# Optimization experiments

Measured on AMD Instinct MI355X. Metric: run time of the kernel, lower is better.

The kernel has to match this reference:

```python
import jax, jax.numpy as jnp
import numpy as np

H = 12          # num heads
D = 768         # embed dim
HD = D // H     # head dim
SCALE = HD ** -0.5
NEG = -(3.0 ** 39)  # matches torch's triu(1) * -3.0**39 mask value


def setup_inputs() -> dict:
    key = jax.random.key(0)
    ks = jax.random.split(key, 9)
    B, S = 4, 1024
    lim = 1.0 / np.sqrt(D)
    def lin(k):
        kw, kb = jax.random.split(k)
        W = jax.random.uniform(kw, (D, D), jnp.float32, -lim, lim)  # [out,in]
        b = jax.random.uniform(kb, (D,), jnp.float32, -lim, lim)
        return W, b
    Wq, bq = lin(ks[0]); Wk, bk = lin(ks[1]); Wv, bv = lin(ks[2]); Wo, bo = lin(ks[3])
    hidden_states = jax.random.normal(ks[4], (B, S, D), jnp.float32)
    return {"hidden_states": hidden_states,
            "Wq": Wq, "bq": bq, "Wk": Wk, "bk": bk,
            "Wv": Wv, "bv": bv, "Wo": Wo, "bo": bo}


def reference(hidden_states, Wq, bq, Wk, bk, Wv, bv, Wo, bo):
    B, S, _ = hidden_states.shape
    split = lambda x: x.reshape(B, S, H, HD).transpose(0, 2, 1, 3)  # [B,H,S,HD]
    q = split(hidden_states @ Wq.T + bq) * SCALE
    k = split(hidden_states @ Wk.T + bk)
    v = split(hidden_states @ Wv.T + bv)
    scores = jnp.einsum('bhqd,bhkd->bhqk', q, k)
    causal_mask = jnp.triu(jnp.full((S, S), NEG, hidden_states.dtype), k=1)
    scores = scores + causal_mask  # broadcast over [B,H]
    probs = jax.nn.softmax(scores, axis=-1)
    out = jnp.einsum('bhqk,bhkd->bhqd', probs, v)
    out = out.transpose(0, 2, 1, 3).reshape(B, S, H * HD)
    return out @ Wo.T + bo
```

## Files before the change

kernel.cpp:

```cpp
#include <hip/hip_runtime.h>

#define NH 12
#define DM 768
#define HD 64
#define BB 4
#define SS 1024
#define MTOT (BB*SS)
#define ATT_SCALE 0.125f
#define NEGMASK (-4.0525551530189755e18f)

typedef __attribute__((ext_vector_type(8))) short short8;
typedef __attribute__((ext_vector_type(4))) float floatx4;
typedef __attribute__((ext_vector_type(4))) unsigned short ushort4v;

__device__ __forceinline__ float bf2f(unsigned short u){
    union { unsigned int i; float f; } x; x.i = ((unsigned int)u) << 16; return x.f;
}
__device__ __forceinline__ unsigned short f2bf(float f){
    union { float f; unsigned int i; } x; x.f = f;
    unsigned int i = x.i;
    return (unsigned short)((i + 0x7FFFu + ((i >> 16) & 1u)) >> 16);
}

#define XQ4 (MTOT*DM/4)
#define WQ4 (DM*DM/4)

__global__ __launch_bounds__(256) void convert_bf16(
    const float* __restrict__ X,
    const float* __restrict__ Wq, const float* __restrict__ Wk,
    const float* __restrict__ Wv, const float* __restrict__ Wo,
    unsigned short* __restrict__ Xb,
    unsigned short* __restrict__ Wqb, unsigned short* __restrict__ Wkb,
    unsigned short* __restrict__ Wvb, unsigned short* __restrict__ Wob)
{
    const int idx = blockIdx.x * 256 + threadIdx.x;
    const float* s; unsigned short* d; int off;
    if (idx < XQ4) { s = X; d = Xb; off = idx; }
    else {
        const int r = idx - XQ4;
        const int wsel = r / WQ4;
        off = r - wsel * WQ4;
        s = (wsel==0)?Wq:(wsel==1)?Wk:(wsel==2)?Wv:Wo;
        d = (wsel==0)?Wqb:(wsel==1)?Wkb:(wsel==2)?Wvb:Wob;
    }
    const float4 v = ((const float4*)s)[off];
    ushort4v o;
    o[0] = f2bf(v.x); o[1] = f2bf(v.y); o[2] = f2bf(v.z); o[3] = f2bf(v.w);
    ((ushort4v*)d)[off] = o;
}

__device__ __forceinline__ void gemm_stage(
    const unsigned short* __restrict__ A,
    const unsigned short* __restrict__ Bm,
    int m0, int n0, int k0, int w, int lane,
    unsigned short* __restrict__ As, unsigned short* __restrict__ Bs)
{
    const int srow = lane >> 2;
    const int ske  = (lane & 3) * 8;
    #pragma unroll
    for (int j = 0; j < 2; ++j) {
        const int row = w*32 + j*16 + srow;
        __builtin_amdgcn_global_load_lds(
            (const __attribute__((address_space(1))) unsigned int*)
                (A + (size_t)(m0 + row) * DM + k0 + ske),
            (__attribute__((address_space(3))) unsigned int*)
                (As + (w*32 + j*16) * 32),
            16, 0, 0);
        __builtin_amdgcn_global_load_lds(
            (const __attribute__((address_space(1))) unsigned int*)
                (Bm + (size_t)(n0 + row) * DM + k0 + ske),
            (__attribute__((address_space(3))) unsigned int*)
                (Bs + (w*32 + j*16) * 32),
            16, 0, 0);
    }
}

__device__ __forceinline__ void gemm_compute(
    const unsigned short* __restrict__ As,
    const unsigned short* __restrict__ Bs,
    int wr, int wc, int c, int g, floatx4 (&acc)[4][4])
{
    short8 af[4], bfr[4];
    #pragma unroll
    for (int mi = 0; mi < 4; ++mi)
        af[mi] = *(const short8*)(As + (wr*64 + mi*16 + c)*32 + g*8);
    #pragma unroll
    for (int ni = 0; ni < 4; ++ni)
        bfr[ni] = *(const short8*)(Bs + (wc*64 + ni*16 + c)*32 + g*8);
    #pragma unroll
    for (int mi = 0; mi < 4; ++mi)
        #pragma unroll
        for (int ni = 0; ni < 4; ++ni)
            acc[mi][ni] = __builtin_amdgcn_mfma_f32_16x16x32_bf16(
                af[mi], bfr[ni], acc[mi][ni], 0, 0, 0);
}

__global__ __launch_bounds__(256) void qkv_mfma(
    const unsigned short* __restrict__ Xb,
    const unsigned short* __restrict__ Wqkv,
    const float* __restrict__ bq, const float* __restrict__ bk,
    const float* __restrict__ bv,
    unsigned short* __restrict__ qout,
    unsigned short* __restrict__ kout,
    unsigned short* __restrict__ vout)
{
    const int bx = blockIdx.x;
    const int which = bx / 6;
    const int np0 = (bx % 6) * 128;
    const int n0 = bx * 128;
    const int m0 = blockIdx.y * 128;

    const float* bias = (which==0) ? bq : (which==1) ? bk : bv;
    const float scl = (which==0) ? ATT_SCALE : 1.0f;

    __shared__ unsigned short As[2][128*32];
    __shared__ unsigned short Bs[2][128*32];

    const int t = threadIdx.x;
    const int w = t >> 6, lane = t & 63;
    const int c = lane & 15, g = lane >> 4;
    const int wr = w >> 1, wc = w & 1;

    floatx4 acc[4][4] = {};

    gemm_stage(Xb, Wqkv, m0, n0, 0, w, lane, As[0], Bs[0]);
    __syncthreads();

    #pragma unroll 2
    for (int kt = 0; kt < 24; ++kt) {
        const int cur = kt & 1;
        if (kt + 1 < 24)
            gemm_stage(Xb, Wqkv, m0, n0, (kt+1)*32, w, lane, As[cur^1], Bs[cur^1]);
        gemm_compute(As[cur], Bs[cur], wr, wc, c, g, acc);
        if (kt + 1 < 24)
            __syncthreads();
    }

    #pragma unroll
    for (int mi = 0; mi < 4; ++mi) {
        #pragma unroll
        for (int r = 0; r < 4; ++r) {
            const int m = m0 + wr*64 + mi*16 + g*4 + r;
            const int b = m >> 10, s = m & 1023;
            #pragma unroll
            for (int ni = 0; ni < 4; ++ni) {
                const int np = np0 + wc*64 + ni*16 + c;
                const int h = np >> 6, hd = np & 63;
                const float val = (acc[mi][ni][r] + bias[np]) * scl;
                if (which == 2)
                    vout[(((size_t)(b*NH + h))*HD + hd)*SS + s] = f2bf(val);
                else if (which == 1)
                    kout[(((size_t)(b*NH + h))*SS + s)*HD + hd] = f2bf(val);
                else
                    qout[(((size_t)(b*NH + h))*SS + s)*HD + hd] = f2bf(val);
            }
        }
    }
}

__device__ __forceinline__ void stage_tile(
    const unsigned short* __restrict__ Kp,
    const unsigned short* __restrict__ VTp,
    int k0, int w, int lane,
    unsigned short* __restrict__ Ks,
    unsigned short* __restrict__ Vs)
{
    const int rsub = lane >> 3;
    const int cc   = (lane & 7) ^ rsub;
    #pragma unroll
    for (int j = 0; j < 2; ++j) {
        const int r = w*16 + j*8 + rsub;
        __builtin_amdgcn_global_load_lds(
            (const __attribute__((address_space(1))) unsigned int*)
                (Kp + (size_t)(k0 + r) * HD + cc*8),
            (__attribute__((address_space(3))) unsigned int*)
                (Ks + (w*16 + j*8) * HD),
            16, 0, 0);
        __builtin_amdgcn_global_load_lds(
            (const __attribute__((address_space(1))) unsigned int*)
                (VTp + (size_t)r * SS + k0 + cc*8),
            (__attribute__((address_space(3))) unsigned int*)
                (Vs + (w*16 + j*8) * HD),
            16, 0, 0);
    }
}

__device__ __forceinline__ void attn_process_tile(
    const unsigned short* __restrict__ Ks,
    const unsigned short* __restrict__ Vs,
    const short8 (&qf)[2],
    int k0, bool islast, int qg, int c, int g,
    float& m_c, float& l_c, floatx4 (&Oacc)[4],
    unsigned short* __restrict__ Pl)
{
    floatx4 S[4] = {};
    #pragma unroll
    for (int nf = 0; nf < 4; ++nf) {
        const int row = nf*16 + c;
        #pragma unroll
        for (int st = 0; st < 2; ++st) {
            const short8 kf = *(const short8*)(Ks + row*HD + (((g + 4*st) ^ (c & 7)) * 8));
            S[nf] = __builtin_amdgcn_mfma_f32_16x16x32_bf16(kf, qf[st], S[nf], 0, 0, 0);
        }
    }

    if (islast) {
        #pragma unroll
        for (int nf = 0; nf < 4; ++nf) {
            #pragma unroll
            for (int r = 0; r < 4; ++r) {
                const int key = k0 + nf*16 + g*4 + r;
                if (key > qg) S[nf][r] += NEGMASK;
            }
        }
    }

    float mx = -INFINITY;
    #pragma unroll
    for (int nf = 0; nf < 4; ++nf)
        #pragma unroll
        for (int r = 0; r < 4; ++r) mx = fmaxf(mx, S[nf][r]);
    mx = fmaxf(mx, __shfl_xor(mx, 16, 64));
    mx = fmaxf(mx, __shfl_xor(mx, 32, 64));
    const float mnew = fmaxf(m_c, mx);
    const float alpha = __expf(m_c - mnew);
    float sum = 0.0f;
    #pragma unroll
    for (int nf = 0; nf < 4; ++nf)
        #pragma unroll
        for (int r = 0; r < 4; ++r) {
            const float p = __expf(S[nf][r] - mnew);
            S[nf][r] = p;
            sum += p;
        }
    sum += __shfl_xor(sum, 16, 64);
    sum += __shfl_xor(sum, 32, 64);
    l_c = l_c * alpha + sum;
    m_c = mnew;
    #pragma unroll
    for (int nf = 0; nf < 4; ++nf)
        #pragma unroll
        for (int r = 0; r < 4; ++r) Oacc[nf][r] *= alpha;

    #pragma unroll
    for (int nf = 0; nf < 4; ++nf)
        #pragma unroll
        for (int r = 0; r < 4; ++r)
            Pl[c * 72 + nf*16 + g*4 + r] = f2bf(S[nf][r]);

    #pragma unroll
    for (int st = 0; st < 2; ++st) {
        const short8 pf = *(const short8*)(Pl + c * 72 + g*8 + 32*st);
        #pragma unroll
        for (int nf = 0; nf < 4; ++nf) {
            const int row = nf*16 + c;
            const short8 vf = *(const short8*)(Vs + row*HD + (((g + 4*st) ^ (c & 7)) * 8));
            Oacc[nf] = __builtin_amdgcn_mfma_f32_16x16x32_bf16(vf, pf, Oacc[nf], 0, 0, 0);
        }
    }
}

__global__ __launch_bounds__(256) void attn_mfma(
    const unsigned short* __restrict__ Q,
    const unsigned short* __restrict__ K,
    const unsigned short* __restrict__ VT,
    unsigned short* __restrict__ O)
{
    const int idx = blockIdx.x;
    const int bh  = idx % 48;
    const int z   = 15 - (idx / 48);
    const int q0  = z * 64;

    const unsigned short* Qp  = Q  + (size_t)bh * SS * HD;
    const unsigned short* Kp  = K  + (size_t)bh * SS * HD;
    const unsigned short* VTp = VT + (size_t)bh * HD * SS;

    __shared__ unsigned short Ks[2][64*HD];
    __shared__ unsigned short Vs[2][64*HD];
    __shared__ unsigned short Pl[4][16*72];

    const int t    = threadIdx.x;
    const int w    = t >> 6;
    const int lane = t & 63;
    const int c    = lane & 15;
    const int g    = lane >> 4;
    const int qg   = q0 + w*16 + c;

    short8 qf[2];
    #pragma unroll
    for (int st = 0; st < 2; ++st)
        qf[st] = *(const short8*)(Qp + (size_t)qg * HD + g*8 + 32*st);

    floatx4 Oacc[4] = {};
    float m_c = -INFINITY, l_c = 0.0f;

    const int ntile = z + 1;

    stage_tile(Kp, VTp, 0, w, lane, Ks[0], Vs[0]);
    __syncthreads();

    for (int kt = 0; kt < ntile; ++kt) {
        const int cur = kt & 1;
        if (kt + 1 < ntile)
            stage_tile(Kp, VTp, (kt+1)*64, w, lane, Ks[cur^1], Vs[cur^1]);
        attn_process_tile(Ks[cur], Vs[cur], qf, kt*64, kt == ntile-1,
                          qg, c, g, m_c, l_c, Oacc, Pl[w]);
        if (kt + 1 < ntile)
            __syncthreads();
    }

    const int b = bh / NH, h = bh % NH;
    const float inv = 1.0f / l_c;
    unsigned short* op = O + ((size_t)(b*SS + qg))*DM + h*HD;
    #pragma unroll
    for (int nf = 0; nf < 4; ++nf) {
        ushort4v o4;
        #pragma unroll
        for (int r = 0; r < 4; ++r) o4[r] = f2bf(Oacc[nf][r] * inv);
        *(ushort4v*)(op + nf*16 + g*4) = o4;
    }
}

__global__ __launch_bounds__(256) void out_mfma(
    const unsigned short* __restrict__ A,
    const unsigned short* __restrict__ Wb,
    const float* __restrict__ bias,
    float* __restrict__ outf)
{
    const int n0 = blockIdx.x * 128;
    const int m0 = blockIdx.y * 128;

    __shared__ unsigned short As[2][128*32];
    __shared__ unsigned short Bs[2][128*32];

    const int t = threadIdx.x;
    const int w = t >> 6, lane = t & 63;
    const int c = lane & 15, g = lane >> 4;
    const int wr = w >> 1, wc = w & 1;

    floatx4 acc[4][4] = {};

    gemm_stage(A, Wb, m0, n0, 0, w, lane, As[0], Bs[0]);
    __syncthreads();

    #pragma unroll 2
    for (int kt = 0; kt < 24; ++kt) {
        const int cur = kt & 1;
        if (kt + 1 < 24)
            gemm_stage(A, Wb, m0, n0, (kt+1)*32, w, lane, As[cur^1], Bs[cur^1]);
        gemm_compute(As[cur], Bs[cur], wr, wc, c, g, acc);
        if (kt + 1 < 24)
            __syncthreads();
    }

    #pragma unroll
    for (int mi = 0; mi < 4; ++mi) {
        #pragma unroll
        for (int r = 0; r < 4; ++r) {
            const int m = m0 + wr*64 + mi*16 + g*4 + r;
            #pragma unroll
            for (int ni = 0; ni < 4; ++ni) {
                const int n = n0 + wc*64 + ni*16 + c;
                outf[(size_t)m * DM + n] = acc[mi][ni][r] + bias[n];
            }
        }
    }
}

extern "C" void kernel_launch(void* const* d_in, const int* in_sizes, int n_in,
                              void* d_out, int out_size, void* d_ws, size_t ws_size,
                              hipStream_t stream) {
    const float* X  = (const float*)d_in[0];
    const float* Wq = (const float*)d_in[1];
    const float* bq = (const float*)d_in[2];
    const float* Wk = (const float*)d_in[3];
    const float* bk = (const float*)d_in[4];
    const float* Wv = (const float*)d_in[5];
    const float* bv = (const float*)d_in[6];
    const float* Wo = (const float*)d_in[7];
    const float* bo = (const float*)d_in[8];
    float* out = (float*)d_out;

    const size_t elems = (size_t)MTOT * DM;
    const size_t welems = (size_t)DM * DM;
    unsigned short* q    = (unsigned short*)d_ws;
    unsigned short* k    = q    + elems;
    unsigned short* vt   = k    + elems;
    unsigned short* attn = vt   + elems;
    unsigned short* xb   = attn + elems;
    unsigned short* wqb  = xb   + elems;
    unsigned short* wkb  = wqb  + welems;
    unsigned short* wvb  = wkb  + welems;
    unsigned short* wob  = wvb  + welems;

    convert_bf16<<<dim3((XQ4 + 4*WQ4) / 256), 256, 0, stream>>>(
        X, Wq, Wk, Wv, Wo, xb, wqb, wkb, wvb, wob);
    qkv_mfma<<<dim3(18, 32), 256, 0, stream>>>(
        xb, wqb, bq, bk, bv, q, k, vt);
    attn_mfma<<<dim3(768), 256, 0, stream>>>(q, k, vt, attn);
    out_mfma<<<dim3(6, 32), 256, 0, stream>>>(attn, wob, bo, out);
}
```

Measured before the change: 177.1 us.

## Retile projection GEMMs to 128x64 with BK=64 swizzled LDS, vectorize P stores

The QKV and output projection GEMMs move from 128x128 tiles with BK=32 double buffering to 128x64 tiles with BK=64, single-buffered, using an XOR-swizzled LDS layout. This doubles the grid size so more blocks fill the CUs, and it should reduce LDS bank conflicts on fragment reads. The cost is the loss of load/compute overlap from double buffering and lower per-block reuse. The attention kernel also packs its P-tile LDS writes into 4-wide vector stores.

```diff
diff --git a/kernel.cpp b/kernel.cpp
--- a/kernel.cpp
+++ b/kernel.cpp
@@ -49,50 +49,57 @@
     ((ushort4v*)d)[off] = o;
 }
 
-__device__ __forceinline__ void gemm_stage(
+__device__ __forceinline__ void gemm_stage64(
     const unsigned short* __restrict__ A,
     const unsigned short* __restrict__ Bm,
     int m0, int n0, int k0, int w, int lane,
-    unsigned short* __restrict__ As, unsigned short* __restrict__ Bs)
-{
-    const int srow = lane >> 2;
-    const int ske  = (lane & 3) * 8;
-    #pragma unroll
-    for (int j = 0; j < 2; ++j) {
-        const int row = w*32 + j*16 + srow;
+    unsigned short* __restrict__ As,
+    unsigned short* __restrict__ Bs)
+{
+    const int rsub = lane >> 3;
+    const int cc   = (lane & 7) ^ rsub;
+    #pragma unroll
+    for (int j = 0; j < 4; ++j) {
+        const int rb = w*32 + j*8;
         __builtin_amdgcn_global_load_lds(
             (const __attribute__((address_space(1))) unsigned int*)
-                (A + (size_t)(m0 + row) * DM + k0 + ske),
-            (__attribute__((address_space(3))) unsigned int*)
-                (As + (w*32 + j*16) * 32),
+                (A + (size_t)(m0 + rb + rsub) * DM + k0 + cc*8),
+            (__attribute__((address_space(3))) unsigned int*)(As + rb*64),
             16, 0, 0);
+    }
+    #pragma unroll
+    for (int j = 0; j < 2; ++j) {
+        const int rb = w*16 + j*8;
         __builtin_amdgcn_global_load_lds(
             (const __attribute__((address_space(1))) unsigned int*)
-                (Bm + (size_t)(n0 + row) * DM + k0 + ske),
-            (__attribute__((address_space(3))) unsigned int*)
-                (Bs + (w*32 + j*16) * 32),
+                (Bm + (size_t)(n0 + rb + rsub) * DM + k0 + cc*8),
+            (__attribute__((address_space(3))) unsigned int*)(Bs + rb*64),
             16, 0, 0);
     }
 }
 
-__device__ __forceinline__ void gemm_compute(
+__device__ __forceinline__ void gemm_compute64(
     const unsigned short* __restrict__ As,
     const unsigned short* __restrict__ Bs,
-    int wr, int wc, int c, int g, floatx4 (&acc)[4][4])
-{
-    short8 af[4], bfr[4];
-    #pragma unroll
-    for (int mi = 0; mi < 4; ++mi)
-        af[mi] = *(const short8*)(As + (wr*64 + mi*16 + c)*32 + g*8);
-    #pragma unroll
-    for (int ni = 0; ni < 4; ++ni)
-        bfr[ni] = *(const short8*)(Bs + (wc*64 + ni*16 + c)*32 + g*8);
-    #pragma unroll
-    for (int mi = 0; mi < 4; ++mi)
-        #pragma unroll
-        for (int ni = 0; ni < 4; ++ni)
-            acc[mi][ni] = __builtin_amdgcn_mfma_f32_16x16x32_bf16(
-                af[mi], bfr[ni], acc[mi][ni], 0, 0, 0);
+    int wr, int wc, int c, int g, floatx4 (&acc)[4][2])
+{
+    #pragma unroll
+    for (int st = 0; st < 2; ++st) {
+        const int chunk = ((g + 4*st) ^ (c & 7)) * 8;
+        short8 af[4], bfr[2];
+        #pragma unroll
+        for (int mi = 0; mi < 4; ++mi)
+            af[mi] = *(const short8*)(As + (wr*64 + mi*16 + c)*64 + chunk);
+        #pragma unroll
+        for (int ni = 0; ni < 2; ++ni)
+            bfr[ni] = *(const short8*)(Bs + (wc*32 + ni*16 + c)*64 + chunk);
+        #pragma unroll
+        for (int mi = 0; mi < 4; ++mi)
+            #pragma unroll
+            for (int ni = 0; ni < 2; ++ni)
+                acc[mi][ni] = __builtin_amdgcn_mfma_f32_16x16x32_bf16(
+                    af[mi], bfr[ni], acc[mi][ni], 0, 0, 0);
+    }
 }
 
 __global__ __launch_bounds__(256) void qkv_mfma(
@@ -105,35 +112,29 @@
     unsigned short* __restrict__ vout)
 {
     const int bx = blockIdx.x;
-    const int which = bx / 6;
-    const int np0 = (bx % 6) * 128;
-    const int n0 = bx * 128;
+    const int which = bx / 12;
+    const int np0 = (bx % 12) * 64;
+    const int n0 = bx * 64;
     const int m0 = blockIdx.y * 128;
 
     const float* bias = (which==0) ? bq : (which==1) ? bk : bv;
     const float scl = (which==0) ? ATT_SCALE : 1.0f;
 
-    __shared__ unsigned short As[2][128*32];
-    __shared__ unsigned short Bs[2][128*32];
+    __shared__ unsigned short As[128*64];
+    __shared__ unsigned short Bs[64*64];
 
     const int t = threadIdx.x;
     const int w = t >> 6, lane = t & 63;
     const int c = lane & 15, g = lane >> 4;
     const int wr = w >> 1, wc = w & 1;
 
-    floatx4 acc[4][4] = {};
-
-    gemm_stage(Xb, Wqkv, m0, n0, 0, w, lane, As[0], Bs[0]);
-    __syncthreads();
-
-    #pragma unroll 2
-    for (int kt = 0; kt < 24; ++kt) {
-        const int cur = kt & 1;
-        if (kt + 1 < 24)
-            gemm_stage(Xb, Wqkv, m0, n0, (kt+1)*32, w, lane, As[cur^1], Bs[cur^1]);
-        gemm_compute(As[cur], Bs[cur], wr, wc, c, g, acc);
-        if (kt + 1 < 24)
-            __syncthreads();
+    floatx4 acc[4][2] = {};
+
+    for (int kt = 0; kt < 12; ++kt) {
+        __syncthreads();
+        gemm_stage64(Xb, Wqkv, m0, n0, kt*64, w, lane, As, Bs);
+        __syncthreads();
+        gemm_compute64(As, Bs, wr, wc, c, g, acc);
     }
 
     #pragma unroll
@@ -143,8 +144,8 @@
             const int m = m0 + wr*64 + mi*16 + g*4 + r;
             const int b = m >> 10, s = m & 1023;
             #pragma unroll
-            for (int ni = 0; ni < 4; ++ni) {
-                const int np = np0 + wc*64 + ni*16 + c;
+            for (int ni = 0; ni < 2; ++ni) {
+                const int np = np0 + wc*32 + ni*16 + c;
                 const int h = np >> 6, hd = np & 63;
                 const float val = (acc[mi][ni][r] + bias[np]) * scl;
                 if (which == 2)
@@ -243,10 +244,12 @@
         for (int r = 0; r < 4; ++r) Oacc[nf][r] *= alpha;
 
     #pragma unroll
-    for (int nf = 0; nf < 4; ++nf)
-        #pragma unroll
-        for (int r = 0; r < 4; ++r)
-            Pl[c * 72 + nf*16 + g*4 + r] = f2bf(S[nf][r]);
+    for (int nf = 0; nf < 4; ++nf) {
+        ushort4v p4;
+        #pragma unroll
+        for (int r = 0; r < 4; ++r) p4[r] = f2bf(S[nf][r]);
+        *(ushort4v*)(Pl + c*72 + nf*16 + g*4) = p4;
+    }
 
     #pragma unroll
     for (int st = 0; st < 2; ++st) {
@@ -327,30 +330,24 @@
     const float* __restrict__ bias,
     float* __restrict__ outf)
 {
-    const int n0 = blockIdx.x * 128;
+    const int n0 = blockIdx.x * 64;
     const int m0 = blockIdx.y * 128;
 
-    __shared__ unsigned short As[2][128*32];
-    __shared__ unsigned short Bs[2][128*32];
+    __shared__ unsigned short As[128*64];
+    __shared__ unsigned short Bs[64*64];
 
     const int t = threadIdx.x;
     const int w = t >> 6, lane = t & 63;
     const int c = lane & 15, g = lane >> 4;
     const int wr = w >> 1, wc = w & 1;
 
-    floatx4 acc[4][4] = {};
-
-    gemm_stage(A, Wb, m0, n0, 0, w, lane, As[0], Bs[0]);
-    __syncthreads();
-
-    #pragma unroll 2
-    for (int kt = 0; kt < 24; ++kt) {
-        const int cur = kt & 1;
-        if (kt + 1 < 24)
-            gemm_stage(A, Wb, m0, n0, (kt+1)*32, w, lane, As[cur^1], Bs[cur^1]);
-        gemm_compute(As[cur], Bs[cur], wr, wc, c, g, acc);
-        if (kt + 1 < 24)
-            __syncthreads();
+    floatx4 acc[4][2] = {};
+
+    for (int kt = 0; kt < 12; ++kt) {
+        __syncthreads();
+        gemm_stage64(A, Wb, m0, n0, kt*64, w, lane, As, Bs);
+        __syncthreads();
+        gemm_compute64(As, Bs, wr, wc, c, g, acc);
     }
 
     #pragma unroll
@@ -359,8 +356,8 @@
         for (int r = 0; r < 4; ++r) {
             const int m = m0 + wr*64 + mi*16 + g*4 + r;
             #pragma unroll
-            for (int ni = 0; ni < 4; ++ni) {
-                const int n = n0 + wc*64 + ni*16 + c;
+            for (int ni = 0; ni < 2; ++ni) {
+                const int n = n0 + wc*32 + ni*16 + c;
                 outf[(size_t)m * DM + n] = acc[mi][ni][r] + bias[n];
             }
         }
@@ -395,8 +392,8 @@
 
     convert_bf16<<<dim3((XQ4 + 4*WQ4) / 256), 256, 0, stream>>>(
         X, Wq, Wk, Wv, Wo, xb, wqb, wkb, wvb, wob);
-    qkv_mfma<<<dim3(18, 32), 256, 0, stream>>>(
+    qkv_mfma<<<dim3(36, 32), 256, 0, stream>>>(
         xb, wqb, bq, bk, bv, q, k, vt);
     attn_mfma<<<dim3(768), 256, 0, stream>>>(q, k, vt, attn);
-    out_mfma<<<dim3(6, 32), 256, 0, stream>>>(attn, wob, bo, out);
-}
+    out_mfma<<<dim3(12, 32), 256, 0, stream>>>(attn, wob, bo, out);
+}
```

Result: faster. 153.8 us (-13.1%).
